# Optimization experiments

Hardware: AMD Instinct MI355X
Metric: run time of the kernel (lower is better)

The kernel has to match this reference:

```python
import jax, jax.numpy as jnp
import numpy as np

B, N, G, K, C = 16, 8192, 128, 32, 384
EPS = 1e-5


def _fps(xyz, n):
    # furthest point sampling starting at index 0 (matches pointnet2 CUDA op)
    b = xyz.shape[0]
    dists = jnp.sum((xyz - xyz[:, :1]) ** 2, -1)  # [B,N] dist^2 to first pt

    def step(d, _):
        idx = jnp.argmax(d, axis=-1)                       # [B]
        p = jnp.take_along_axis(xyz, idx[:, None, None], 1)  # [B,1,3]
        d = jnp.minimum(d, jnp.sum((xyz - p) ** 2, -1))
        return d, idx.astype(jnp.int32)

    _, idxs = jax.lax.scan(step, dists, None, length=n - 1)
    idx = jnp.concatenate([jnp.zeros((1, b), jnp.int32), idxs], 0).T  # [B,n]
    return jnp.take_along_axis(xyz, idx[..., None], axis=1)


def _morton_order(center):
    # greedy nearest-neighbour tour over group centers (simplied_morton_sorting)
    b, g, _ = center.shape
    d = jnp.sum((center[:, :, None] - center[:, None]) ** 2, -1)  # [B,G,G]
    d = jnp.where(jnp.eye(g, dtype=bool), jnp.inf, d)

    def step(carry, _):
        cur, visited = carry
        row = jnp.take_along_axis(d, cur[:, None, None], 1)[:, 0]  # [B,G]
        row = jnp.where(visited, jnp.inf, row)
        nxt = jnp.argmin(row, -1).astype(jnp.int32)
        visited = visited | jax.nn.one_hot(nxt, g, dtype=bool)
        return (nxt, visited), nxt

    cur0 = jnp.zeros((b,), jnp.int32)
    init = (cur0, jax.nn.one_hot(cur0, g, dtype=bool))
    _, nxts = jax.lax.scan(step, init, None, length=g - 1)
    return jnp.concatenate([jnp.zeros((1, b), jnp.int32), nxts], 0).T  # [B,G]


def _bn(x, g_, b_, m_, v_):
    return (x - m_) * (g_ * jax.lax.rsqrt(v_ + EPS)) + b_


def _pos_embed(center):
    npf = 128  # 384 // 3 // 2 * 2
    i = jnp.arange(npf, dtype=jnp.float32)
    dim_t = 10000.0 ** (2.0 * jnp.floor(i / 2) / npf)
    x = center * (2.0 * np.pi)
    pd = x[..., None] / dim_t                                # [B,G,3,128]
    emb = jnp.stack([jnp.sin(pd[..., 0::2]), jnp.cos(pd[..., 1::2])], -1)
    return emb.reshape(*center.shape[:-1], -1)               # [B,G,384]


def _forward(xyz, w1, b1, g1, bt1, m1, v1, w2, b2, w3, b3, g3, bt3, m3, v3, w4, b4):
    center = _fps(xyz, G)                                    # [B,G,3]
    # squared-distance KNN (argsort order identical to euclidean cdist)
    d2 = (jnp.sum(center ** 2, -1)[:, :, None]
          + jnp.sum(xyz ** 2, -1)[:, None]
          - 2.0 * jnp.einsum('bgd,bnd->bgn', center, xyz))   # [B,G,N]
    _, idx = jax.lax.top_k(-d2, K)                           # [B,G,K]
    neigh = jnp.take_along_axis(xyz, idx.reshape(B, G * K)[..., None], 1)
    neigh = neigh.reshape(B, G, K, 3) - center[:, :, None]
    order = _morton_order(center)                            # [B,G]
    neigh = jnp.take_along_axis(neigh, order[:, :, None, None], 1)
    center = jnp.take_along_axis(center, order[:, :, None], 1)
    # Encoder_small (1x1 convs == per-point linears, eval-mode BN)
    pg = neigh.reshape(B * G, K, 3)
    f = jax.nn.relu(_bn(pg @ w1.T + b1, g1, bt1, m1, v1)) @ w2.T + b2  # [BG,K,256]
    fg = jnp.max(f, 1, keepdims=True)
    h = jnp.concatenate([jnp.broadcast_to(fg, f.shape), f], -1)        # [BG,K,512]
    h = jax.nn.relu(_bn(h @ w3.T + b3, g3, bt3, m3, v3)) @ w4.T + b4   # [BG,K,384]
    tokens = jnp.max(h, 1).reshape(B, G, C)
    return tokens + _pos_embed(center)


def setup_inputs() -> dict:
    key = jax.random.key(0)
    ks = jax.random.split(key, 8)
    s = 0.05
    return {
        'xyz': jax.random.normal(ks[0], (B, N, 3), jnp.float32),
        'w1': jax.random.normal(ks[1], (128, 3), jnp.float32) * s,
        'b1': jax.random.normal(ks[2], (128,), jnp.float32) * s,
        'g1': jnp.ones((128,), jnp.float32),
        'bt1': jnp.zeros((128,), jnp.float32),
        'm1': jnp.zeros((128,), jnp.float32),
        'v1': jnp.ones((128,), jnp.float32),
        'w2': jax.random.normal(ks[3], (256, 128), jnp.float32) * s,
        'b2': jax.random.normal(ks[4], (256,), jnp.float32) * s,
        'w3': jax.random.normal(ks[5], (512, 512), jnp.float32) * s,
        'b3': jnp.zeros((512,), jnp.float32),
        'g3': jnp.ones((512,), jnp.float32),
        'bt3': jnp.zeros((512,), jnp.float32),
        'm3': jnp.zeros((512,), jnp.float32),
        'v3': jnp.ones((512,), jnp.float32),
        'w4': jax.random.normal(ks[6], (384, 512), jnp.float32) * s,
        'b4': jax.random.normal(ks[7], (384,), jnp.float32) * s,
    }


def reference(xyz, w1, b1, g1, bt1, m1, v1, w2, b2, w3, b3, g3, bt3, m3, v3, w4, b4):
    return _forward(xyz, w1, b1, g1, bt1, m1, v1, w2, b2, w3, b3, g3, bt3, m3, v3, w4, b4)
```

## Files before the change

kernel.cpp:

```cpp
#include <hip/hip_runtime.h>
#include <hip/hip_bf16.h>

#define B_ 16
#define N_ 8192
#define G_ 128
#define K_ 32
#define C_ 384
#define EPSV 1e-5f

typedef __attribute__((ext_vector_type(8))) short bf16x8;
typedef __attribute__((ext_vector_type(8))) unsigned short u16x8;
typedef __attribute__((ext_vector_type(4))) float f32x4;
typedef __attribute__((ext_vector_type(2))) float f32x2;

__device__ __forceinline__ unsigned short f2b(float f){
  unsigned int u = __float_as_uint(f);
  u += 0x7fffu + ((u >> 16) & 1u);
  return (unsigned short)(u >> 16);
}
__device__ __forceinline__ float b2f(unsigned short s){
  return __uint_as_float(((unsigned int)s) << 16);
}
__device__ __forceinline__ float sq3(float dx, float dy, float dz){
  return __fadd_rn(__fadd_rn(__fmul_rn(dx,dx), __fmul_rn(dy,dy)), __fmul_rn(dz,dz));
}
__device__ __forceinline__ f32x2 pkmax(f32x2 a, f32x2 b){
  return f32x2{fmaxf(a.x,b.x), fmaxf(a.y,b.y)};
}
__device__ __forceinline__ unsigned fenc(float f){
  unsigned u = __float_as_uint(f);
  return ((int)u >= 0) ? (u | 0x80000000u) : ~u;
}

#define DPP_MAXU_STAGE(r, CTRL) { \
  unsigned _o = (unsigned)__builtin_amdgcn_update_dpp((int)(r), (int)(r), (CTRL), 0xf, 0xf, false); \
  (r) = ((r) > _o) ? (r) : _o; }
#define DPP_MAXU_ALL(r) \
  DPP_MAXU_STAGE(r, 0x111) DPP_MAXU_STAGE(r, 0x112) DPP_MAXU_STAGE(r, 0x114) \
  DPP_MAXU_STAGE(r, 0x118) DPP_MAXU_STAGE(r, 0x142) DPP_MAXU_STAGE(r, 0x143)
#define DPP_MINU_STAGE(r, CTRL) { \
  unsigned _o = (unsigned)__builtin_amdgcn_update_dpp((int)(r), (int)(r), (CTRL), 0xf, 0xf, false); \
  (r) = ((r) < _o) ? (r) : _o; }
#define DPP_MINU_ALL(r) \
  DPP_MINU_STAGE(r, 0x111) DPP_MINU_STAGE(r, 0x112) DPP_MINU_STAGE(r, 0x114) \
  DPP_MINU_STAGE(r, 0x118) DPP_MINU_STAGE(r, 0x142) DPP_MINU_STAGE(r, 0x143)

__global__ __launch_bounds__(256) void prep_kernel(
    const float* __restrict__ w2, const float* __restrict__ w3,
    const float* __restrict__ w4, unsigned short* __restrict__ w2b,
    unsigned short* __restrict__ w3b, unsigned short* __restrict__ w4b){
  int i = blockIdx.x*256 + threadIdx.x;
  if (i < 32768){ w2b[i] = f2b(w2[i]); return; }
  i -= 32768;
  if (i < 262144){ w3b[i] = f2b(w3[i]); return; }
  i -= 262144;
  if (i < 196608){ w4b[i] = f2b(w4[i]); }
}

__attribute__((amdgpu_flat_work_group_size(256,256), amdgpu_waves_per_eu(1,1)))
__global__ void fps_morton_kernel(const float* __restrict__ xyz,
                                  float* __restrict__ centers_ord){
  const int b = blockIdx.x, t = threadIdx.x, w = t >> 6;
  const int lane = t & 63;
  const float* xb = xyz + (size_t)b*N_*3;
  __shared__ __align__(16) float sval[2][4];
  __shared__ __align__(16) int   sidx[2][4];
  __shared__ float clx[G_], cly[G_], clz[G_];
  const int base = t*32;
  f32x2 X[16], Y[16], Z[16], D[16];
  f32x2 mmax;
  const float p0x = xb[0], p0y = xb[1], p0z = xb[2];
  {
#pragma clang fp contract(off)
    float s[96];
    const float4* src = (const float4*)(xb + (size_t)base*3);
    #pragma unroll
    for (int q = 0; q < 24; q++) ((float4*)s)[q] = src[q];
    mmax = f32x2{-1.f, -1.f};
    #pragma unroll
    for (int p = 0; p < 16; p++){
      X[p] = f32x2{s[6*p+0], s[6*p+3]};
      Y[p] = f32x2{s[6*p+1], s[6*p+4]};
      Z[p] = f32x2{s[6*p+2], s[6*p+5]};
      const f32x2 dx = X[p] - p0x, dy = Y[p] - p0y, dz = Z[p] - p0z;
      D[p] = (dx*dx + dy*dy) + dz*dz;
      mmax = pkmax(mmax, D[p]);
    }
  }
  if (t == 0){ clx[0] = p0x; cly[0] = p0y; clz[0] = p0z; }
  int buf = 0;
  for (int g = 1; g < G_; g++){
    const float v = fmaxf(mmax.x, mmax.y);
    int jl = 0;
    #pragma unroll
    for (int p = 15; p >= 0; p--){
      if (D[p].y == v) jl = 2*p+1;
      if (D[p].x == v) jl = 2*p;
    }
    const unsigned uv = __float_as_uint(v);
    unsigned r = uv;
    DPP_MAXU_ALL(r)
    const unsigned wmax = (unsigned)__builtin_amdgcn_readlane((int)r, 63);
    const unsigned long long tie = __ballot(uv == wmax);
    const int wl = __ffsll(tie) - 1;
    if (lane == wl){ sval[buf][w] = __uint_as_float(wmax); sidx[buf][w] = base + jl; }
    __syncthreads();
    const float4 vv = *(const float4*)&sval[buf][0];
    const int4   ii = *(const int4*)&sidx[buf][0];
    float bv = vv.x; int bb = ii.x;
    if (vv.y > bv){ bv = vv.y; bb = ii.y; }
    if (vv.z > bv){ bv = vv.z; bb = ii.z; }
    if (vv.w > bv){ bv = vv.w; bb = ii.w; }
    {
#pragma clang fp contract(off)
      const int ubb = __builtin_amdgcn_readfirstlane(bb);
      const float cx = xb[ubb*3], cy = xb[ubb*3+1], cz = xb[ubb*3+2];
      if (t == 0){ clx[g] = cx; cly[g] = cy; clz[g] = cz; }
      mmax = f32x2{-1.f, -1.f};
      #pragma unroll
      for (int p = 0; p < 16; p++){
        const f32x2 dx = X[p] - cx, dy = Y[p] - cy, dz = Z[p] - cz;
        const f32x2 dn = (dx*dx + dy*dy) + dz*dz;
        D[p] = f32x2{fminf(D[p].x, dn.x), fminf(D[p].y, dn.y)};
        mmax = pkmax(mmax, D[p]);
      }
    }
    buf ^= 1;
  }
  __syncthreads();
  if (t < 64){
    float mcx[2], mcy[2], mcz[2]; bool mvis[2];
    #pragma unroll
    for (int j = 0; j < 2; j++){
      const int idx = lane + j*64;
      mcx[j] = clx[idx]; mcy[j] = cly[idx]; mcz[j] = clz[idx];
      mvis[j] = (idx == 0);
    }
    float curx = clx[0], cury = cly[0], curz = clz[0];
    if (lane == 0){
      centers_ord[(size_t)b*G_*3 + 0] = curx;
      centers_ord[(size_t)b*G_*3 + 1] = cury;
      centers_ord[(size_t)b*G_*3 + 2] = curz;
    }
    for (int step = 1; step < G_; step++){
      const float d0r = sq3(__fsub_rn(mcx[0],curx), __fsub_rn(mcy[0],cury), __fsub_rn(mcz[0],curz));
      const float d1r = sq3(__fsub_rn(mcx[1],curx), __fsub_rn(mcy[1],cury), __fsub_rn(mcz[1],curz));
      const float d0 = mvis[0] ? __builtin_inff() : d0r;
      const float d1 = mvis[1] ? __builtin_inff() : d1r;
      float mv = d0; int mi = lane;
      if (d1 < mv){ mv = d1; mi = lane + 64; }
      const int wj = mi >> 6;
      const float sx = wj ? mcx[1] : mcx[0];
      const float sy = wj ? mcy[1] : mcy[0];
      const float sz = wj ? mcz[1] : mcz[0];
      const unsigned key = __float_as_uint(mv);
      unsigned r = key;
      DPP_MINU_ALL(r)
      const unsigned wmin = (unsigned)__builtin_amdgcn_readlane((int)r, 63);
      const unsigned long long tie = __ballot(key == wmin);
      int wl;
      if (__popcll(tie) == 1){
        wl = __ffsll(tie) - 1;
      } else {
        float tv = mv; int ti = mi;
        #pragma unroll
        for (int mk = 1; mk < 64; mk <<= 1){
          const float ov = __shfl_xor(tv, mk);
          const int   oi = __shfl_xor(ti, mk);
          if (ov < tv || (ov == tv && oi < ti)){ tv = ov; ti = oi; }
        }
        wl = ti & 63;
      }
      const int mbi = __builtin_amdgcn_readlane(mi, wl);
      curx = __uint_as_float((unsigned)__builtin_amdgcn_readlane((int)__float_as_uint(sx), wl));
      cury = __uint_as_float((unsigned)__builtin_amdgcn_readlane((int)__float_as_uint(sy), wl));
      curz = __uint_as_float((unsigned)__builtin_amdgcn_readlane((int)__float_as_uint(sz), wl));
      if (lane == wl){
        if ((mbi >> 6) == 0) mvis[0] = true; else mvis[1] = true;
      }
      if (lane == 0){
        centers_ord[((size_t)b*G_ + step)*3 + 0] = curx;
        centers_ord[((size_t)b*G_ + step)*3 + 1] = cury;
        centers_ord[((size_t)b*G_ + step)*3 + 2] = curz;
      }
    }
  }
}

__global__ __launch_bounds__(256, 2) void knn_kernel(const float* __restrict__ xyz,
                                                     const float* __restrict__ centers_ord,
                                                     float* __restrict__ neigh){
  const int gp = blockIdx.x, b = blockIdx.y, t = threadIdx.x;
  const int lane = t & 63, w = t >> 6;
  __shared__ __align__(16) float sv[2][4];
  __shared__ __align__(16) int   si[2][4];
  __shared__ int list[K_];
  const float* xb = xyz + (size_t)b*N_*3;
  const float* cp = centers_ord + ((size_t)b*G_ + gp)*3;
  const float cxv = cp[0], cyv = cp[1], czv = cp[2];
  const float cc = sq3(cxv, cyv, czv);
  const int base = t*32;
  float dd[32];
  float v = __builtin_inff(); int jl = 0;
  {
    float s[96];
    const float4* src = (const float4*)(xb + (size_t)base*3);
    #pragma unroll
    for (int q = 0; q < 24; q++) ((float4*)s)[q] = src[q];
    #pragma unroll
    for (int j = 0; j < 32; j++){
      const float x = s[3*j], y = s[3*j+1], z = s[3*j+2];
      const float xx = sq3(x, y, z);
      const float dot = __fadd_rn(__fadd_rn(__fmul_rn(cxv,x), __fmul_rn(cyv,y)), __fmul_rn(czv,z));
      dd[j] = __fsub_rn(__fadd_rn(cc, xx), __fmul_rn(2.f, dot));
      if (dd[j] < v){ v = dd[j]; jl = j; }
    }
  }
  int buf = 0;
  for (int it = 0; it < K_; it++){
    const unsigned key = fenc(v);
    unsigned r = key;
    DPP_MINU_ALL(r)
    const unsigned wmin = (unsigned)__builtin_amdgcn_readlane((int)r, 63);
    const unsigned long long tie = __ballot(key == wmin);
    const int wl = __ffsll(tie) - 1;
    if (lane == wl){ sv[buf][w] = v; si[buf][w] = base + jl; }
    __syncthreads();
    const float4 vv = *(const float4*)&sv[buf][0];
    const int4   ii = *(const int4*)&si[buf][0];
    float bv = vv.x; int bb = ii.x;
    if (vv.y < bv){ bv = vv.y; bb = ii.y; }
    if (vv.z < bv){ bv = vv.z; bb = ii.z; }
    if (vv.w < bv){ bv = vv.w; bb = ii.w; }
    if (t == 0) list[it] = bb;
    if ((bb >> 5) == t){
      const int jw = bb & 31;
      #pragma unroll
      for (int j = 0; j < 32; j++) if (j == jw) dd[j] = __builtin_inff();
      v = __builtin_inff(); jl = 0;
      #pragma unroll
      for (int j = 0; j < 32; j++) if (dd[j] < v){ v = dd[j]; jl = j; }
    }
    buf ^= 1;
  }
  __syncthreads();
  if (t < K_*3){
    const int k = t / 3, d = t % 3;
    const int n = list[k];
    neigh[(((size_t)b*G_ + gp)*K_ + k)*3 + d] = __fsub_rn(xb[n*3+d], cp[d]);
  }
}

__device__ __forceinline__ int swzA1(int row, int col){
  int byteo = row*256 + col*2;
  byteo ^= (row & 7) << 4;
  return byteo >> 1;
}
__device__ __forceinline__ int swzF(int row, int col){
  int byteo = row*512 + col*2;
  byteo ^= (row & 7) << 4;
  return byteo >> 1;
}
__device__ __forceinline__ int swzA(int row, int col){
  int byteo = row*1024 + col*2;
  byteo ^= (row & 7) << 4;
  return byteo >> 1;
}

#define NG3 3

__global__ __launch_bounds__(512, 2) void enc_kernel(
    const float* __restrict__ neigh, const float* __restrict__ centers_ord,
    const float* __restrict__ w1, const float* __restrict__ b1,
    const float* __restrict__ g1, const float* __restrict__ bt1,
    const float* __restrict__ m1, const float* __restrict__ v1,
    const unsigned short* __restrict__ w2b, const float* __restrict__ b2,
    const unsigned short* __restrict__ w3b, const float* __restrict__ b3,
    const float* __restrict__ g3, const float* __restrict__ bt3,
    const float* __restrict__ m3, const float* __restrict__ v3,
    const unsigned short* __restrict__ w4b, const float* __restrict__ b4,
    float* __restrict__ out)
{
  const int t = threadIdx.x;
  const int lane = t & 63, w = t >> 6, lr = lane & 15, lg = lane >> 4;
  const int gid0 = blockIdx.x*NG3;
  const int ng = min(NG3, 2048 - gid0);
  __shared__ __align__(16) char smem[148992];
  unsigned short* A3s = (unsigned short*)smem;
  unsigned short* A1s = (unsigned short*)smem;
  unsigned short* Flp = (unsigned short*)(smem + 98304);
  unsigned short* fgb = (unsigned short*)(smem + 147456);
  float* tokp = (float*)(smem + 98304);

  for (int it = t; it < NG3*256; it += 512){
    const int g = it >> 8, rem = it & 255, p = rem >> 3, c0 = (rem & 7) * 16;
    const float* pgp = neigh + (size_t)(gid0 + g)*96 + p*3;
    const float px = pgp[0], py = pgp[1], pz = pgp[2];
    unsigned short hv[16];
    #pragma unroll
    for (int cc = 0; cc < 16; cc++){
      const int c = c0 + cc;
      const float wx = w1[c*3], wy = w1[c*3+1], wz = w1[c*3+2];
      const float sc = g1[c] * rsqrtf(v1[c] + EPSV);
      float val = px*wx + py*wy + pz*wz + b1[c];
      val = (val - m1[c])*sc + bt1[c];
      hv[cc] = f2b(fmaxf(val, 0.f));
    }
    *(u16x8*)&A1s[g*4096 + swzA1(p, c0)]     = *(u16x8*)&hv[0];
    *(u16x8*)&A1s[g*4096 + swzA1(p, c0 + 8)] = *(u16x8*)&hv[8];
  }
  __syncthreads();

  {
    const int col0 = w*32;
    f32x4 acc[2][NG3][2];
    #pragma unroll
    for (int nt = 0; nt < 2; nt++)
      #pragma unroll
      for (int g = 0; g < NG3; g++)
        #pragma unroll
        for (int m = 0; m < 2; m++){ f32x4 z = {0.f,0.f,0.f,0.f}; acc[nt][g][m] = z; }
    #pragma unroll
    for (int kt = 0; kt < 4; kt++){
      bf16x8 bA[NG3][2];
      #pragma unroll
      for (int g = 0; g < NG3; g++)
        #pragma unroll
        for (int m = 0; m < 2; m++)
          bA[g][m] = *(const bf16x8*)&A1s[g*4096 + swzA1(m*16 + lr, kt*32 + lg*8)];
      bf16x8 bB[2];
      #pragma unroll
      for (int nt = 0; nt < 2; nt++)
        bB[nt] = *(const bf16x8*)(w2b + (size_t)(col0 + nt*16 + lr)*128 + kt*32 + lg*8);
      #pragma unroll
      for (int nt = 0; nt < 2; nt++)
        #pragma unroll
        for (int g = 0; g < NG3; g++)
          #pragma unroll
          for (int m = 0; m < 2; m++)
            acc[nt][g][m] = __builtin_amdgcn_mfma_f32_16x16x32_bf16(bA[g][m], bB[nt], acc[nt][g][m], 0,0,0);
    }
    #pragma unroll
    for (int nt = 0; nt < 2; nt++){
      const int col = col0 + nt*16 + lr;
      const float bc = b2[col];
      #pragma unroll
      for (int g = 0; g < NG3; g++)
        #pragma unroll
        for (int m = 0; m < 2; m++)
          #pragma unroll
          for (int r = 0; r < 4; r++)
            Flp[g*8192 + swzF(m*16 + lg*4 + r, col)] = f2b(acc[nt][g][m][r] + bc);
    }
  }
  __syncthreads();

  for (int it = t; it < NG3*256; it += 512){
    const int g = it >> 8, col = it & 255;
    float mx = -__builtin_inff();
    #pragma unroll 4
    for (int row = 0; row < 32; row++) mx = fmaxf(mx, b2f(Flp[g*8192 + swzF(row, col)]));
    fgb[g*256 + col] = f2b(mx);
  }
  __syncthreads();

  {
    const int col0 = w*64;
    f32x4 acc[4][NG3][2];
    #pragma unroll
    for (int nt = 0; nt < 4; nt++)
      #pragma unroll
      for (int g = 0; g < NG3; g++)
        #pragma unroll
        for (int m = 0; m < 2; m++){ f32x4 z = {0.f,0.f,0.f,0.f}; acc[nt][g][m] = z; }
    #pragma unroll
    for (int kt = 0; kt < 16; kt++){
      bf16x8 bA[NG3][2];
      if (kt < 8){
        #pragma unroll
        for (int g = 0; g < NG3; g++){
          const bf16x8 af = *(const bf16x8*)&fgb[g*256 + kt*32 + lg*8];
          bA[g][0] = af; bA[g][1] = af;
        }
      } else {
        #pragma unroll
        for (int g = 0; g < NG3; g++)
          #pragma unroll
          for (int m = 0; m < 2; m++)
            bA[g][m] = *(const bf16x8*)&Flp[g*8192 + swzF(m*16 + lr, (kt-8)*32 + lg*8)];
      }
      bf16x8 bB[4];
      #pragma unroll
      for (int nt = 0; nt < 4; nt++)
        bB[nt] = *(const bf16x8*)(w3b + (size_t)(col0 + nt*16 + lr)*512 + kt*32 + lg*8);
      #pragma unroll
      for (int nt = 0; nt < 4; nt++)
        #pragma unroll
        for (int g = 0; g < NG3; g++)
          #pragma unroll
          for (int m = 0; m < 2; m++)
            acc[nt][g][m] = __builtin_amdgcn_mfma_f32_16x16x32_bf16(bA[g][m], bB[nt], acc[nt][g][m], 0,0,0);
    }
    #pragma unroll
    for (int nt = 0; nt < 4; nt++){
      const int col = col0 + nt*16 + lr;
      const float bc = b3[col];
      const float sc = g3[col]*rsqrtf(v3[col] + EPSV);
      const float mm = m3[col], bb = bt3[col];
      #pragma unroll
      for (int g = 0; g < NG3; g++)
        #pragma unroll
        for (int m = 0; m < 2; m++)
          #pragma unroll
          for (int r = 0; r < 4; r++){
            float val = acc[nt][g][m][r] + bc;
            val = (val - mm)*sc + bb;
            A3s[g*16384 + swzA(m*16 + lg*4 + r, col)] = f2b(fmaxf(val, 0.f));
          }
    }
  }
  __syncthreads();

  {
    const int col0 = w*48;
    f32x4 acc[3][NG3][2];
    #pragma unroll
    for (int nt = 0; nt < 3; nt++)
      #pragma unroll
      for (int g = 0; g < NG3; g++)
        #pragma unroll
        for (int m = 0; m < 2; m++){ f32x4 z = {0.f,0.f,0.f,0.f}; acc[nt][g][m] = z; }
    #pragma unroll
    for (int kt = 0; kt < 16; kt++){
      bf16x8 bA[NG3][2];
      #pragma unroll
      for (int g = 0; g < NG3; g++)
        #pragma unroll
        for (int m = 0; m < 2; m++)
          bA[g][m] = *(const bf16x8*)&A3s[g*16384 + swzA(m*16 + lr, kt*32 + lg*8)];
      bf16x8 bB[3];
      #pragma unroll
      for (int nt = 0; nt < 3; nt++)
        bB[nt] = *(const bf16x8*)(w4b + (size_t)(col0 + nt*16 + lr)*512 + kt*32 + lg*8);
      #pragma unroll
      for (int nt = 0; nt < 3; nt++)
        #pragma unroll
        for (int g = 0; g < NG3; g++)
          #pragma unroll
          for (int m = 0; m < 2; m++)
            acc[nt][g][m] = __builtin_amdgcn_mfma_f32_16x16x32_bf16(bA[g][m], bB[nt], acc[nt][g][m], 0,0,0);
    }
    #pragma unroll
    for (int nt = 0; nt < 3; nt++){
      const int col = col0 + nt*16 + lr;
      const float bc = b4[col];
      #pragma unroll
      for (int g = 0; g < NG3; g++){
        float mx = fmaxf(
          fmaxf(fmaxf(acc[nt][g][0][0], acc[nt][g][0][1]), fmaxf(acc[nt][g][0][2], acc[nt][g][0][3])),
          fmaxf(fmaxf(acc[nt][g][1][0], acc[nt][g][1][1]), fmaxf(acc[nt][g][1][2], acc[nt][g][1][3])));
        mx = fmaxf(mx, __shfl_xor(mx, 16));
        mx = fmaxf(mx, __shfl_xor(mx, 32));
        if (lg == 0) tokp[g*C_ + col] = mx + bc;
      }
    }
  }
  __syncthreads();

  #pragma unroll
  for (int g = 0; g < NG3; g++){
    if (g >= ng) break;
    const int gid = gid0 + g;
    for (int c = t; c < C_; c += 512){
      const int d = c >> 7, r = c & 127, m2 = r >> 1;
      const float e = (float)(2*m2) * (1.f/128.f);
      const float dimt = powf(10000.f, e);
      const float ctrd = centers_ord[(size_t)gid*3 + d];
      const float x2 = __fmul_rn(ctrd, 6.28318530717958647692f);
      const float ang = __fdiv_rn(x2, dimt);
      out[(size_t)gid*C_ + c] = tokp[g*C_ + c] + ((r & 1) ? cosf(ang) : sinf(ang));
    }
  }
}

extern "C" void kernel_launch(void* const* d_in, const int* in_sizes, int n_in,
                              void* d_out, int out_size, void* d_ws, size_t ws_size,
                              hipStream_t stream){
  (void)in_sizes; (void)n_in; (void)out_size; (void)ws_size;
  const float* xyz = (const float*)d_in[0];
  const float* w1  = (const float*)d_in[1];
  const float* b1  = (const float*)d_in[2];
  const float* g1  = (const float*)d_in[3];
  const float* bt1 = (const float*)d_in[4];
  const float* m1  = (const float*)d_in[5];
  const float* v1  = (const float*)d_in[6];
  const float* w2  = (const float*)d_in[7];
  const float* b2  = (const float*)d_in[8];
  const float* w3  = (const float*)d_in[9];
  const float* b3  = (const float*)d_in[10];
  const float* g3  = (const float*)d_in[11];
  const float* bt3 = (const float*)d_in[12];
  const float* m3  = (const float*)d_in[13];
  const float* v3  = (const float*)d_in[14];
  const float* w4  = (const float*)d_in[15];
  const float* b4  = (const float*)d_in[16];

  char* ws = (char*)d_ws;
  float* centers_ord  = (float*)(ws + 24576);
  float* neigh        = (float*)(ws + 49152);
  unsigned short* w2b = (unsigned short*)(ws + 835584);
  unsigned short* w3b = (unsigned short*)(ws + 901120);
  unsigned short* w4b = (unsigned short*)(ws + 1425408);

  prep_kernel      <<<1920, 256, 0, stream>>>(w2, w3, w4, w2b, w3b, w4b);
  fps_morton_kernel<<<B_, 256, 0, stream>>>(xyz, centers_ord);
  knn_kernel       <<<dim3(G_, B_), 256, 0, stream>>>(xyz, centers_ord, neigh);
  enc_kernel       <<<683, 512, 0, stream>>>(neigh, centers_ord,
      w1, b1, g1, bt1, m1, v1, w2b, b2, w3b, b3, g3, bt3, m3, v3, w4b, b4,
      (float*)d_out);
}
```

Baseline: 478.4 us.

## Merge weight conversion into FPS launch and double-buffer MLP weight fragment loads

```diff
diff --git a/kernel.cpp b/kernel.cpp
--- a/kernel.cpp
+++ b/kernel.cpp
@@ -45,22 +45,26 @@
   DPP_MINU_STAGE(r, 0x111) DPP_MINU_STAGE(r, 0x112) DPP_MINU_STAGE(r, 0x114) \
   DPP_MINU_STAGE(r, 0x118) DPP_MINU_STAGE(r, 0x142) DPP_MINU_STAGE(r, 0x143)
 
-__global__ __launch_bounds__(256) void prep_kernel(
-    const float* __restrict__ w2, const float* __restrict__ w3,
-    const float* __restrict__ w4, unsigned short* __restrict__ w2b,
-    unsigned short* __restrict__ w3b, unsigned short* __restrict__ w4b){
-  int i = blockIdx.x*256 + threadIdx.x;
-  if (i < 32768){ w2b[i] = f2b(w2[i]); return; }
-  i -= 32768;
-  if (i < 262144){ w3b[i] = f2b(w3[i]); return; }
-  i -= 262144;
-  if (i < 196608){ w4b[i] = f2b(w4[i]); }
-}
-
 __attribute__((amdgpu_flat_work_group_size(256,256), amdgpu_waves_per_eu(1,1)))
-__global__ void fps_morton_kernel(const float* __restrict__ xyz,
-                                  float* __restrict__ centers_ord){
-  const int b = blockIdx.x, t = threadIdx.x, w = t >> 6;
+__global__ void fps_morton_prep_kernel(const float* __restrict__ xyz,
+                                       float* __restrict__ centers_ord,
+                                       const float* __restrict__ w2f,
+                                       const float* __restrict__ w3f,
+                                       const float* __restrict__ w4f,
+                                       unsigned short* __restrict__ w2b,
+                                       unsigned short* __restrict__ w3b,
+                                       unsigned short* __restrict__ w4b){
+  const int t = threadIdx.x;
+  if (blockIdx.x >= B_){
+    int i = (blockIdx.x - B_)*256 + t;
+    if (i < 32768){ w2b[i] = f2b(w2f[i]); return; }
+    i -= 32768;
+    if (i < 262144){ w3b[i] = f2b(w3f[i]); return; }
+    i -= 262144;
+    if (i < 196608) w4b[i] = f2b(w4f[i]);
+    return;
+  }
+  const int b = blockIdx.x, w = t >> 6;
   const int lane = t & 63;
   const float* xb = xyz + (size_t)b*N_*3;
   __shared__ __align__(16) float sval[2][4];
@@ -373,34 +377,54 @@
       for (int g = 0; g < NG3; g++)
         #pragma unroll
         for (int m = 0; m < 2; m++){ f32x4 z = {0.f,0.f,0.f,0.f}; acc[nt][g][m] = z; }
-    #pragma unroll
-    for (int kt = 0; kt < 16; kt++){
-      bf16x8 bA[NG3][2];
-      if (kt < 8){
-        #pragma unroll
-        for (int g = 0; g < NG3; g++){
-          const bf16x8 af = *(const bf16x8*)&fgb[g*256 + kt*32 + lg*8];
-          bA[g][0] = af; bA[g][1] = af;
+    bf16x8 bB0[4], bB1[4];
+    #pragma unroll
+    for (int nt = 0; nt < 4; nt++)
+      bB0[nt] = *(const bf16x8*)(w3b + (size_t)(col0 + nt*16 + lr)*512 + lg*8);
+
+#define L3_BODY(KT, BBC) { \
+    bf16x8 bA[NG3][2]; \
+    if ((KT) < 8){ \
+      _Pragma("unroll") \
+      for (int g = 0; g < NG3; g++){ \
+        const bf16x8 af = *(const bf16x8*)&fgb[g*256 + (KT)*32 + lg*8]; \
+        bA[g][0] = af; bA[g][1] = af; \
+      } \
+    } else { \
+      _Pragma("unroll") \
+      for (int g = 0; g < NG3; g++) \
+        _Pragma("unroll") \
+        for (int m = 0; m < 2; m++) \
+          bA[g][m] = *(const bf16x8*)&Flp[g*8192 + swzF(m*16 + lr, ((KT)-8)*32 + lg*8)]; \
+    } \
+    _Pragma("unroll") \
+    for (int nt = 0; nt < 4; nt++) \
+      _Pragma("unroll") \
+      for (int g = 0; g < NG3; g++) \
+        _Pragma("unroll") \
+        for (int m = 0; m < 2; m++) \
+          acc[nt][g][m] = __builtin_amdgcn_mfma_f32_16x16x32_bf16(bA[g][m], (BBC)[nt], acc[nt][g][m], 0,0,0); }
+
+    #pragma unroll
+    for (int kp = 0; kp < 8; kp++){
+      {
+        const int kt = 2*kp;
+        #pragma unroll
+        for (int nt = 0; nt < 4; nt++)
+          bB1[nt] = *(const bf16x8*)(w3b + (size_t)(col0 + nt*16 + lr)*512 + (kt+1)*32 + lg*8);
+        L3_BODY(kt, bB0)
+      }
+      {
+        const int kt = 2*kp + 1;
+        if (kt < 15){
+          #pragma unroll
+          for (int nt = 0; nt < 4; nt++)
+            bB0[nt] = *(const bf16x8*)(w3b + (size_t)(col0 + nt*16 + lr)*512 + (kt+1)*32 + lg*8);
         }
-      } else {
-        #pragma unroll
-        for (int g = 0; g < NG3; g++)
-          #pragma unroll
-          for (int m = 0; m < 2; m++)
-            bA[g][m] = *(const bf16x8*)&Flp[g*8192 + swzF(m*16 + lr, (kt-8)*32 + lg*8)];
-      }
-      bf16x8 bB[4];
-      #pragma unroll
-      for (int nt = 0; nt < 4; nt++)
-        bB[nt] = *(const bf16x8*)(w3b + (size_t)(col0 + nt*16 + lr)*512 + kt*32 + lg*8);
-      #pragma unroll
-      for (int nt = 0; nt < 4; nt++)
-        #pragma unroll
-        for (int g = 0; g < NG3; g++)
-          #pragma unroll
-          for (int m = 0; m < 2; m++)
-            acc[nt][g][m] = __builtin_amdgcn_mfma_f32_16x16x32_bf16(bA[g][m], bB[nt], acc[nt][g][m], 0,0,0);
-    }
+        L3_BODY(kt, bB1)
+      }
+    }
+#undef L3_BODY
     #pragma unroll
     for (int nt = 0; nt < 4; nt++){
       const int col = col0 + nt*16 + lr;
@@ -430,26 +454,46 @@
       for (int g = 0; g < NG3; g++)
         #pragma unroll
         for (int m = 0; m < 2; m++){ f32x4 z = {0.f,0.f,0.f,0.f}; acc[nt][g][m] = z; }
-    #pragma unroll
-    for (int kt = 0; kt < 16; kt++){
-      bf16x8 bA[NG3][2];
-      #pragma unroll
-      for (int g = 0; g < NG3; g++)
-        #pragma unroll
-        for (int m = 0; m < 2; m++)
-          bA[g][m] = *(const bf16x8*)&A3s[g*16384 + swzA(m*16 + lr, kt*32 + lg*8)];
-      bf16x8 bB[3];
-      #pragma unroll
-      for (int nt = 0; nt < 3; nt++)
-        bB[nt] = *(const bf16x8*)(w4b + (size_t)(col0 + nt*16 + lr)*512 + kt*32 + lg*8);
-      #pragma unroll
-      for (int nt = 0; nt < 3; nt++)
-        #pragma unroll
-        for (int g = 0; g < NG3; g++)
+    bf16x8 bB0[3], bB1[3];
+    #pragma unroll
+    for (int nt = 0; nt < 3; nt++)
+      bB0[nt] = *(const bf16x8*)(w4b + (size_t)(col0 + nt*16 + lr)*512 + lg*8);
+
+#define L4_BODY(KT, BBC) { \
+    bf16x8 bA[NG3][2]; \
+    _Pragma("unroll") \
+    for (int g = 0; g < NG3; g++) \
+      _Pragma("unroll") \
+      for (int m = 0; m < 2; m++) \
+        bA[g][m] = *(const bf16x8*)&A3s[g*16384 + swzA(m*16 + lr, (KT)*32 + lg*8)]; \
+    _Pragma("unroll") \
+    for (int nt = 0; nt < 3; nt++) \
+      _Pragma("unroll") \
+      for (int g = 0; g < NG3; g++) \
+        _Pragma("unroll") \
+        for (int m = 0; m < 2; m++) \
+          acc[nt][g][m] = __builtin_amdgcn_mfma_f32_16x16x32_bf16(bA[g][m], (BBC)[nt], acc[nt][g][m], 0,0,0); }
+
+    #pragma unroll
+    for (int kp = 0; kp < 8; kp++){
+      {
+        const int kt = 2*kp;
+        #pragma unroll
+        for (int nt = 0; nt < 3; nt++)
+          bB1[nt] = *(const bf16x8*)(w4b + (size_t)(col0 + nt*16 + lr)*512 + (kt+1)*32 + lg*8);
+        L4_BODY(kt, bB0)
+      }
+      {
+        const int kt = 2*kp + 1;
+        if (kt < 15){
           #pragma unroll
-          for (int m = 0; m < 2; m++)
-            acc[nt][g][m] = __builtin_amdgcn_mfma_f32_16x16x32_bf16(bA[g][m], bB[nt], acc[nt][g][m], 0,0,0);
-    }
+          for (int nt = 0; nt < 3; nt++)
+            bB0[nt] = *(const bf16x8*)(w4b + (size_t)(col0 + nt*16 + lr)*512 + (kt+1)*32 + lg*8);
+        }
+        L4_BODY(kt, bB1)
+      }
+    }
+#undef L4_BODY
     #pragma unroll
     for (int nt = 0; nt < 3; nt++){
       const int col = col0 + nt*16 + lr;
@@ -512,10 +556,10 @@
   unsigned short* w3b = (unsigned short*)(ws + 901120);
   unsigned short* w4b = (unsigned short*)(ws + 1425408);
 
-  prep_kernel      <<<1920, 256, 0, stream>>>(w2, w3, w4, w2b, w3b, w4b);
-  fps_morton_kernel<<<B_, 256, 0, stream>>>(xyz, centers_ord);
-  knn_kernel       <<<dim3(G_, B_), 256, 0, stream>>>(xyz, centers_ord, neigh);
-  enc_kernel       <<<683, 512, 0, stream>>>(neigh, centers_ord,
+  fps_morton_prep_kernel<<<B_ + 1920, 256, 0, stream>>>(xyz, centers_ord,
+      w2, w3, w4, w2b, w3b, w4b);
+  knn_kernel<<<dim3(G_, B_), 256, 0, stream>>>(xyz, centers_ord, neigh);
+  enc_kernel<<<683, 512, 0, stream>>>(neigh, centers_ord,
       w1, b1, g1, bt1, m1, v1, w2b, b2, w3b, b3, g3, bt3, m3, v3, w4b, b4,
       (float*)d_out);
 }
```

New measurement: 482.8 us. No clear change (+0.9%).

## Fuse weight prep into FPS launch, wave-per-group KNN, broadcast FPS coords via LDS

Applied to the files above, without the earlier changes.

```diff
diff --git a/kernel.cpp b/kernel.cpp
--- a/kernel.cpp
+++ b/kernel.cpp
@@ -45,26 +45,31 @@
   DPP_MINU_STAGE(r, 0x111) DPP_MINU_STAGE(r, 0x112) DPP_MINU_STAGE(r, 0x114) \
   DPP_MINU_STAGE(r, 0x118) DPP_MINU_STAGE(r, 0x142) DPP_MINU_STAGE(r, 0x143)
 
-__global__ __launch_bounds__(256) void prep_kernel(
-    const float* __restrict__ w2, const float* __restrict__ w3,
-    const float* __restrict__ w4, unsigned short* __restrict__ w2b,
-    unsigned short* __restrict__ w3b, unsigned short* __restrict__ w4b){
-  int i = blockIdx.x*256 + threadIdx.x;
-  if (i < 32768){ w2b[i] = f2b(w2[i]); return; }
-  i -= 32768;
-  if (i < 262144){ w3b[i] = f2b(w3[i]); return; }
-  i -= 262144;
-  if (i < 196608){ w4b[i] = f2b(w4[i]); }
-}
-
 __attribute__((amdgpu_flat_work_group_size(256,256), amdgpu_waves_per_eu(1,1)))
-__global__ void fps_morton_kernel(const float* __restrict__ xyz,
-                                  float* __restrict__ centers_ord){
-  const int b = blockIdx.x, t = threadIdx.x, w = t >> 6;
+__global__ void fps_morton_prep_kernel(const float* __restrict__ xyz,
+                                       float* __restrict__ centers_ord,
+                                       const float* __restrict__ w2f,
+                                       const float* __restrict__ w3f,
+                                       const float* __restrict__ w4f,
+                                       unsigned short* __restrict__ w2b,
+                                       unsigned short* __restrict__ w3b,
+                                       unsigned short* __restrict__ w4b){
+  const int t = threadIdx.x;
+  if (blockIdx.x >= B_){
+    int i = (blockIdx.x - B_)*256 + t;
+    if (i < 32768){ w2b[i] = f2b(w2f[i]); return; }
+    i -= 32768;
+    if (i < 262144){ w3b[i] = f2b(w3f[i]); return; }
+    i -= 262144;
+    if (i < 196608) w4b[i] = f2b(w4f[i]);
+    return;
+  }
+  const int b = blockIdx.x, w = t >> 6;
   const int lane = t & 63;
   const float* xb = xyz + (size_t)b*N_*3;
-  __shared__ __align__(16) float sval[2][4];
-  __shared__ __align__(16) int   sidx[2][4];
+  __shared__ __align__(16) float  sval[2][4];
+  __shared__ __align__(16) int    sidx[2][4];
+  __shared__ __align__(16) float4 scoord[2][4];
   __shared__ float clx[G_], cly[G_], clz[G_];
   const int base = t*32;
   f32x2 X[16], Y[16], Z[16], D[16];
@@ -103,19 +108,30 @@
     const unsigned wmax = (unsigned)__builtin_amdgcn_readlane((int)r, 63);
     const unsigned long long tie = __ballot(uv == wmax);
     const int wl = __ffsll(tie) - 1;
-    if (lane == wl){ sval[buf][w] = __uint_as_float(wmax); sidx[buf][w] = base + jl; }
+    if (lane == wl){
+      sval[buf][w] = __uint_as_float(wmax); sidx[buf][w] = base + jl;
+      float wx = 0.f, wy = 0.f, wz = 0.f;
+      #pragma unroll
+      for (int p = 0; p < 16; p++)
+        if ((jl >> 1) == p){
+          wx = (jl & 1) ? X[p].y : X[p].x;
+          wy = (jl & 1) ? Y[p].y : Y[p].x;
+          wz = (jl & 1) ? Z[p].y : Z[p].x;
+        }
+      float4 c4; c4.x = wx; c4.y = wy; c4.z = wz; c4.w = 0.f;
+      scoord[buf][w] = c4;
+    }
     __syncthreads();
     const float4 vv = *(const float4*)&sval[buf][0];
-    const int4   ii = *(const int4*)&sidx[buf][0];
-    float bv = vv.x; int bb = ii.x;
-    if (vv.y > bv){ bv = vv.y; bb = ii.y; }
-    if (vv.z > bv){ bv = vv.z; bb = ii.z; }
-    if (vv.w > bv){ bv = vv.w; bb = ii.w; }
+    float bv = vv.x; int q = 0;
+    if (vv.y > bv){ bv = vv.y; q = 1; }
+    if (vv.z > bv){ bv = vv.z; q = 2; }
+    if (vv.w > bv){ bv = vv.w; q = 3; }
+    const float4 c4 = scoord[buf][q];
+    if (t == 0){ clx[g] = c4.x; cly[g] = c4.y; clz[g] = c4.z; }
     {
 #pragma clang fp contract(off)
-      const int ubb = __builtin_amdgcn_readfirstlane(bb);
-      const float cx = xb[ubb*3], cy = xb[ubb*3+1], cz = xb[ubb*3+2];
-      if (t == 0){ clx[g] = cx; cly[g] = cy; clz[g] = cz; }
+      const float cx = c4.x, cy = c4.y, cz = c4.z;
       mmax = f32x2{-1.f, -1.f};
       #pragma unroll
       for (int p = 0; p < 16; p++){
@@ -187,36 +203,42 @@
   }
 }
 
-__global__ __launch_bounds__(256, 2) void knn_kernel(const float* __restrict__ xyz,
-                                                     const float* __restrict__ centers_ord,
-                                                     float* __restrict__ neigh){
-  const int gp = blockIdx.x, b = blockIdx.y, t = threadIdx.x;
-  const int lane = t & 63, w = t >> 6;
-  __shared__ __align__(16) float sv[2][4];
-  __shared__ __align__(16) int   si[2][4];
-  __shared__ int list[K_];
+__attribute__((amdgpu_flat_work_group_size(512,512), amdgpu_waves_per_eu(2,2)))
+__global__ void knn_kernel(const float* __restrict__ xyz,
+                           const float* __restrict__ centers_ord,
+                           float* __restrict__ neigh){
+  const int t = threadIdx.x, lane = t & 63, wv = t >> 6;
+  const int gidx = blockIdx.x*8 + wv;
+  const int b = gidx >> 7, gp = gidx & 127;
   const float* xb = xyz + (size_t)b*N_*3;
   const float* cp = centers_ord + ((size_t)b*G_ + gp)*3;
   const float cxv = cp[0], cyv = cp[1], czv = cp[2];
   const float cc = sq3(cxv, cyv, czv);
-  const int base = t*32;
-  float dd[32];
-  float v = __builtin_inff(); int jl = 0;
-  {
+  const int base = lane*128;
+  float dd[128];
+  float vch[4]; int jch[4];
+  #pragma unroll
+  for (int c = 0; c < 4; c++){
     float s[96];
-    const float4* src = (const float4*)(xb + (size_t)base*3);
+    const float4* src = (const float4*)(xb + (size_t)(base + c*32)*3);
     #pragma unroll
     for (int q = 0; q < 24; q++) ((float4*)s)[q] = src[q];
+    float vc = __builtin_inff(); int jc = 0;
     #pragma unroll
     for (int j = 0; j < 32; j++){
       const float x = s[3*j], y = s[3*j+1], z = s[3*j+2];
       const float xx = sq3(x, y, z);
       const float dot = __fadd_rn(__fadd_rn(__fmul_rn(cxv,x), __fmul_rn(cyv,y)), __fmul_rn(czv,z));
-      dd[j] = __fsub_rn(__fadd_rn(cc, xx), __fmul_rn(2.f, dot));
-      if (dd[j] < v){ v = dd[j]; jl = j; }
-    }
-  }
-  int buf = 0;
+      const float d = __fsub_rn(__fadd_rn(cc, xx), __fmul_rn(2.f, dot));
+      dd[c*32+j] = d;
+      if (d < vc){ vc = d; jc = c*32 + j; }
+    }
+    vch[c] = vc; jch[c] = jc;
+  }
+  float v = vch[0]; int jl = jch[0];
+  #pragma unroll
+  for (int c = 1; c < 4; c++) if (vch[c] < v){ v = vch[c]; jl = jch[c]; }
+  int mybb = 0;
   for (int it = 0; it < K_; it++){
     const unsigned key = fenc(v);
     unsigned r = key;
@@ -224,30 +246,36 @@
     const unsigned wmin = (unsigned)__builtin_amdgcn_readlane((int)r, 63);
     const unsigned long long tie = __ballot(key == wmin);
     const int wl = __ffsll(tie) - 1;
-    if (lane == wl){ sv[buf][w] = v; si[buf][w] = base + jl; }
-    __syncthreads();
-    const float4 vv = *(const float4*)&sv[buf][0];
-    const int4   ii = *(const int4*)&si[buf][0];
-    float bv = vv.x; int bb = ii.x;
-    if (vv.y < bv){ bv = vv.y; bb = ii.y; }
-    if (vv.z < bv){ bv = vv.z; bb = ii.z; }
-    if (vv.w < bv){ bv = vv.w; bb = ii.w; }
-    if (t == 0) list[it] = bb;
-    if ((bb >> 5) == t){
-      const int jw = bb & 31;
-      #pragma unroll
-      for (int j = 0; j < 32; j++) if (j == jw) dd[j] = __builtin_inff();
-      v = __builtin_inff(); jl = 0;
-      #pragma unroll
-      for (int j = 0; j < 32; j++) if (dd[j] < v){ v = dd[j]; jl = j; }
-    }
-    buf ^= 1;
-  }
-  __syncthreads();
-  if (t < K_*3){
-    const int k = t / 3, d = t % 3;
-    const int n = list[k];
-    neigh[(((size_t)b*G_ + gp)*K_ + k)*3 + d] = __fsub_rn(xb[n*3+d], cp[d]);
+    const int bb = __builtin_amdgcn_readlane(base + jl, wl);
+    if (lane == it) mybb = bb;
+    const bool own = (lane == wl);
+    const int jw = bb & 127;
+    const int cb = __builtin_amdgcn_readfirstlane(jw >> 5);
+    const int jj = jw & 31;
+    #pragma unroll
+    for (int c = 0; c < 4; c++){
+      if (cb == c){
+        float vc = __builtin_inff(); int jc = 0;
+        #pragma unroll
+        for (int j = 0; j < 32; j++){
+          float dv = dd[c*32+j];
+          if (own && (j == jj)) dv = __builtin_inff();
+          dd[c*32+j] = dv;
+          if (dv < vc){ vc = dv; jc = c*32 + j; }
+        }
+        vch[c] = vc; jch[c] = jc;
+      }
+    }
+    v = vch[0]; jl = jch[0];
+    #pragma unroll
+    for (int c = 1; c < 4; c++) if (vch[c] < v){ v = vch[c]; jl = jch[c]; }
+  }
+  if (lane < K_){
+    const int n = mybb;
+    float* op = neigh + (((size_t)b*G_ + gp)*K_ + lane)*3;
+    op[0] = __fsub_rn(xb[n*3+0], cxv);
+    op[1] = __fsub_rn(xb[n*3+1], cyv);
+    op[2] = __fsub_rn(xb[n*3+2], czv);
   }
 }
 
@@ -512,10 +540,10 @@
   unsigned short* w3b = (unsigned short*)(ws + 901120);
   unsigned short* w4b = (unsigned short*)(ws + 1425408);
 
-  prep_kernel      <<<1920, 256, 0, stream>>>(w2, w3, w4, w2b, w3b, w4b);
-  fps_morton_kernel<<<B_, 256, 0, stream>>>(xyz, centers_ord);
-  knn_kernel       <<<dim3(G_, B_), 256, 0, stream>>>(xyz, centers_ord, neigh);
-  enc_kernel       <<<683, 512, 0, stream>>>(neigh, centers_ord,
+  fps_morton_prep_kernel<<<B_ + 1920, 256, 0, stream>>>(xyz, centers_ord,
+      w2, w3, w4, w2b, w3b, w4b);
+  knn_kernel<<<256, 512, 0, stream>>>(xyz, centers_ord, neigh);
+  enc_kernel<<<683, 512, 0, stream>>>(neigh, centers_ord,
       w1, b1, g1, bt1, m1, v1, w2b, b2, w3b, b3, g3, bt3, m3, v3, w4b, b4,
       (float*)d_out);
 }
```

Result: slower. 552.7 us (+15.5%).
